# Kernel optimization log

Hardware: AMD Instinct MI355X
Metric: run time of the kernel (lower is better)

The kernel has to match this reference:

```python
import jax, jax.numpy as jnp
import numpy as np

N, E, D = 10000, 160000, 512


def gcn_conv(x, src, dst, W, b):
    # GCNConv (PyG default): linear -> sym-normalized aggregation with self-loops -> +bias
    n = x.shape[0]
    h = x @ W  # [N, D]
    loop = jnp.arange(n)
    s = jnp.concatenate([src, loop])
    d = jnp.concatenate([dst, loop])
    deg = jax.ops.segment_sum(jnp.ones_like(d, dtype=h.dtype), d, num_segments=n)
    dinv = jnp.where(deg > 0, jax.lax.rsqrt(deg), 0.0)
    norm = dinv[s] * dinv[d]  # [E+N]
    msg = h[s] * norm[:, None]  # [E+N, D]
    out = jax.ops.segment_sum(msg, d, num_segments=n)
    return out + b


def gnn_embed(x, edge_index, Ws, bs):
    src, dst = edge_index[0], edge_index[1]
    h = x
    L = len(Ws)
    for i in range(L):
        h = gcn_conv(h, src, dst, Ws[i], bs[i])
        if i < L - 1:
            h = jax.nn.relu(h)
    return jnp.mean(h, axis=0).reshape(1, -1)  # [1, D]


def setup_inputs() -> dict:
    key = jax.random.key(0)
    ks = jax.random.split(key, 16)
    x1 = jax.random.normal(ks[0], (N, D), dtype=jnp.float32)
    x2 = jax.random.normal(ks[1], (N, D), dtype=jnp.float32)
    edge_index1 = jax.random.randint(ks[2], (2, E), 0, N, dtype=jnp.int64)
    edge_index2 = jax.random.randint(ks[3], (2, E), 0, N, dtype=jnp.int64)
    sc = 1.0 / np.sqrt(D)
    W1 = jax.random.normal(ks[4], (D, D), dtype=jnp.float32) * sc
    W2 = jax.random.normal(ks[5], (D, D), dtype=jnp.float32) * sc
    W3 = jax.random.normal(ks[6], (D, D), dtype=jnp.float32) * sc
    b1 = jnp.zeros((D,), jnp.float32)
    b2 = jnp.zeros((D,), jnp.float32)
    b3 = jnp.zeros((D,), jnp.float32)
    # FCL comparison head: concat(u1,u2) [1,2D] -> Linear(2D,D) -> ReLU -> Linear(D,1) -> sigmoid
    Wf1 = jax.random.normal(ks[7], (2 * D, D), dtype=jnp.float32) * (1.0 / np.sqrt(2 * D))
    bf1 = jnp.zeros((D,), jnp.float32)
    Wf2 = jax.random.normal(ks[8], (D, 1), dtype=jnp.float32) * sc
    bf2 = jnp.zeros((1,), jnp.float32)
    return dict(x1=x1, x2=x2, edge_index1=edge_index1, edge_index2=edge_index2,
                W1=W1, W2=W2, W3=W3, b1=b1, b2=b2, b3=b3,
                Wf1=Wf1, bf1=bf1, Wf2=Wf2, bf2=bf2)


def reference(x1, x2, edge_index1, edge_index2, W1, W2, W3, b1, b2, b3, Wf1, bf1, Wf2, bf2):
    Ws, bs = (W1, W2, W3), (b1, b2, b3)
    u1 = gnn_embed(x1, edge_index1, Ws, bs)  # [1, D]
    u2 = gnn_embed(x2, edge_index2, Ws, bs)  # [1, D]
    z = jnp.concatenate([u1, u2], axis=1)  # [1, 2D]
    h = jax.nn.relu(z @ Wf1 + bf1)
    score = jax.nn.sigmoid(h @ Wf2 + bf2)  # [1, 1]
    return score
```

## Files before the change

kernel.cpp:

```cpp
#include <hip/hip_runtime.h>
#include <math.h>

#define NN 10000
#define NE 160000
#define DD 512
#define MPAD 20096

typedef __attribute__((ext_vector_type(8))) short bf16x8;
typedef __attribute__((ext_vector_type(4))) float f32x4;
typedef __attribute__((ext_vector_type(8))) unsigned short u16x8;

__device__ __forceinline__ unsigned short f2bf(float f) {
    unsigned u = __float_as_uint(f);
    u += 0x7FFFu + ((u >> 16) & 1u);
    return (unsigned short)(u >> 16);
}
__device__ __forceinline__ float bf2f(unsigned short h) {
    return __uint_as_float(((unsigned)h) << 16);
}

#define GLOAD16(g, l) __builtin_amdgcn_global_load_lds( \
    (const __attribute__((address_space(1))) void*)(unsigned long long)(const void*)(g), \
    (__attribute__((address_space(3))) void*)(unsigned)(unsigned long long)(void*)(l), \
    16, 0, 0)

__global__ void k_init(int* cnt, int* cursor, float* u, float* hacc) {
    int i = blockIdx.x * blockDim.x + threadIdx.x;
    if (i < 2 * NN) { cnt[i] = 0; cursor[i] = 0; }
    if (i < 2 * DD) u[i] = 0.f;
    if (i < DD) hacc[i] = 0.f;
}

__global__ void k_count(const int* e1, const int* e2, int* cnt) {
    int i = blockIdx.x * blockDim.x + threadIdx.x;
    if (i < NE) {
        atomicAdd(&cnt[e1[NE + i]], 1);
    } else if (i < 2 * NE) {
        int e = i - NE;
        atomicAdd(&cnt[NN + e2[NE + e]], 1);
    }
}

__global__ void k_dinv(const int* cnt, float* dinv) {
    int i = blockIdx.x * blockDim.x + threadIdx.x;
    if (i < 2 * NN) dinv[i] = rsqrtf((float)(cnt[i] + 1));
}

__global__ void k_scan(const int* cnt, int* offs) {
    int g = blockIdx.x;
    const int* c = cnt + g * NN;
    int* o = offs + g * (NN + 1);
    __shared__ int sums[1024];
    int t = threadIdx.x;
    const int PER = 10;
    int base = t * PER;
    int vals[PER];
    int local = 0;
    #pragma unroll
    for (int j = 0; j < PER; ++j) {
        int idx = base + j;
        int v = (idx < NN) ? c[idx] : 0;
        vals[j] = v; local += v;
    }
    sums[t] = local;
    __syncthreads();
    for (int off = 1; off < 1024; off <<= 1) {
        int v = (t >= off) ? sums[t - off] : 0;
        __syncthreads();
        sums[t] += v;
        __syncthreads();
    }
    int prefix = (t > 0) ? sums[t - 1] : 0;
    #pragma unroll
    for (int j = 0; j < PER; ++j) {
        int idx = base + j;
        if (idx < NN) { o[idx] = prefix; prefix += vals[j]; }
    }
    if (t == 1023) o[NN] = sums[1023];
}

__global__ void k_fill(const int* e1, const int* e2, const int* offs,
                       int* cursor, int* adj) {
    int i = blockIdx.x * blockDim.x + threadIdx.x;
    if (i >= 2 * NE) return;
    int g = (i < NE) ? 0 : 1;
    int e = i - g * NE;
    const int* ei = g ? e2 : e1;
    int s = ei[e];
    int d = ei[NE + e];
    int pos = atomicAdd(&cursor[g * NN + d], 1);
    adj[g * NE + offs[g * (NN + 1) + d] + pos] = s;
}

__global__ void k_cvt_x(const float* __restrict__ x1, const float* __restrict__ x2,
                        unsigned short* __restrict__ xb) {
    long long gid = (long long)blockIdx.x * 256 + threadIdx.x;
    long long i8 = gid * 8;
    if (i8 >= (long long)MPAD * DD) return;
    int row = (int)(i8 >> 9);
    int col = (int)(i8 & 511);
    u16x8 ov;
    if (row < 2 * NN) {
        const float* src = (row < NN) ? (x1 + (size_t)row * DD + col)
                                      : (x2 + (size_t)(row - NN) * DD + col);
        float4 f0 = ((const float4*)src)[0];
        float4 f1 = ((const float4*)src)[1];
        ov[0] = f2bf(f0.x); ov[1] = f2bf(f0.y); ov[2] = f2bf(f0.z); ov[3] = f2bf(f0.w);
        ov[4] = f2bf(f1.x); ov[5] = f2bf(f1.y); ov[6] = f2bf(f1.z); ov[7] = f2bf(f1.w);
    } else {
        #pragma unroll
        for (int j = 0; j < 8; ++j) ov[j] = 0;
    }
    *(u16x8*)(xb + i8) = ov;
}

__global__ void k_cvt_w(const float* __restrict__ W1, const float* __restrict__ W2,
                        const float* __restrict__ W3, unsigned short* __restrict__ Wt) {
    __shared__ float t[32][33];
    const float* W = (blockIdx.z == 0) ? W1 : (blockIdx.z == 1) ? W2 : W3;
    unsigned short* o = Wt + (size_t)blockIdx.z * DD * DD;
    int n0 = blockIdx.x * 32, k0 = blockIdx.y * 32;
    int tx = threadIdx.x, ty = threadIdx.y;
    t[ty][tx] = W[(size_t)(k0 + ty) * DD + n0 + tx];
    __syncthreads();
    o[(size_t)(n0 + ty) * DD + k0 + tx] = f2bf(t[tx][ty]);
}

__global__ __launch_bounds__(256) void k_gemm(const unsigned short* __restrict__ A,
                                              const unsigned short* __restrict__ Bt,
                                              unsigned short* __restrict__ C, int M) {
    __shared__ bf16x8 As[512];
    __shared__ bf16x8 Bs[512];
    int tid = threadIdx.x;
    int lane = tid & 63;
    int wid = tid >> 6;
    int wr = wid >> 1, wc = wid & 1;
    int row0 = blockIdx.x * 128;
    int col0 = blockIdx.y * 128;

    int ch0 = wid * 64 + lane;
    int ch1 = 256 + wid * 64 + lane;
    const unsigned short* gA0 = A + (size_t)(row0 + (ch0 & 127)) * DD + (ch0 >> 7) * 8;
    const unsigned short* gA1 = A + (size_t)(row0 + (ch1 & 127)) * DD + (ch1 >> 7) * 8;
    const unsigned short* gB0 = Bt + (size_t)(col0 + (ch0 & 127)) * DD + (ch0 >> 7) * 8;
    const unsigned short* gB1 = Bt + (size_t)(col0 + (ch1 & 127)) * DD + (ch1 >> 7) * 8;

    int iA[4], iB[4];
    #pragma unroll
    for (int m = 0; m < 4; ++m) {
        iA[m] = (lane >> 4) * 128 + wr * 64 + m * 16 + (lane & 15);
        iB[m] = (lane >> 4) * 128 + wc * 64 + m * 16 + (lane & 15);
    }

    f32x4 acc[4][4];
    #pragma unroll
    for (int m = 0; m < 4; ++m)
        #pragma unroll
        for (int n = 0; n < 4; ++n)
            acc[m][n] = (f32x4){0.f, 0.f, 0.f, 0.f};

    for (int k0 = 0; k0 < DD; k0 += 32) {
        GLOAD16(gA0, &As[wid * 64]);
        GLOAD16(gA1, &As[256 + wid * 64]);
        GLOAD16(gB0, &Bs[wid * 64]);
        GLOAD16(gB1, &Bs[256 + wid * 64]);
        gA0 += 32; gA1 += 32; gB0 += 32; gB1 += 32;
        __syncthreads();
        bf16x8 af[4], bfr[4];
        #pragma unroll
        for (int m = 0; m < 4; ++m) { af[m] = As[iA[m]]; bfr[m] = Bs[iB[m]]; }
        #pragma unroll
        for (int m = 0; m < 4; ++m)
            #pragma unroll
            for (int n = 0; n < 4; ++n)
                acc[m][n] = __builtin_amdgcn_mfma_f32_16x16x32_bf16(af[m], bfr[n], acc[m][n], 0, 0, 0);
        __syncthreads();
    }

    #pragma unroll
    for (int m = 0; m < 4; ++m) {
        int rbase = row0 + wr * 64 + m * 16 + (lane >> 4) * 4;
        #pragma unroll
        for (int n = 0; n < 4; ++n) {
            int col = col0 + wc * 64 + n * 16 + (lane & 15);
            f32x4 v = acc[m][n];
            #pragma unroll
            for (int i = 0; i < 4; ++i) {
                int r = rbase + i;
                if (r < M) C[(size_t)r * DD + col] = f2bf(v[i]);
            }
        }
    }
}

template <bool RELU>
__global__ __launch_bounds__(256) void k_aggc(const unsigned short* __restrict__ h,
                                              const int* __restrict__ adj,
                                              const int* __restrict__ offs,
                                              const float* __restrict__ dinv,
                                              const float* __restrict__ bias,
                                              unsigned short* __restrict__ out) {
    int bid = blockIdx.x;
    int combo = bid & 7;
    int nb = bid >> 3;
    int g = combo >> 2;
    int yc = combo & 3;
    int wid = threadIdx.x >> 6;
    int lane = threadIdx.x & 63;
    int sub = lane >> 4;
    int li = lane & 15;
    int v = nb * 16 + wid * 4 + sub;
    int c = yc * 128 + li * 8;
    int gbase = g * NN;
    const int* o = offs + g * (NN + 1);
    int beg = o[v], end = o[v + 1];
    const int* a = adj + g * NE;
    float dv = dinv[gbase + v];
    const unsigned short* hb = h + c;

    u16x8 hv = *(const u16x8*)(hb + (size_t)(gbase + v) * DD);
    float acc[8];
    #pragma unroll
    for (int j = 0; j < 8; ++j) acc[j] = bf2f(hv[j]) * dv;

    int e = beg;
    for (; e + 4 <= end; e += 4) {
        int s0 = a[e] + gbase, s1 = a[e + 1] + gbase;
        int s2 = a[e + 2] + gbase, s3 = a[e + 3] + gbase;
        u16x8 r0 = *(const u16x8*)(hb + (size_t)s0 * DD);
        u16x8 r1 = *(const u16x8*)(hb + (size_t)s1 * DD);
        u16x8 r2 = *(const u16x8*)(hb + (size_t)s2 * DD);
        u16x8 r3 = *(const u16x8*)(hb + (size_t)s3 * DD);
        float d0 = dinv[s0], d1 = dinv[s1], d2 = dinv[s2], d3 = dinv[s3];
        #pragma unroll
        for (int j = 0; j < 8; ++j) {
            acc[j] = fmaf(bf2f(r0[j]), d0, acc[j]);
            acc[j] = fmaf(bf2f(r1[j]), d1, acc[j]);
            acc[j] = fmaf(bf2f(r2[j]), d2, acc[j]);
            acc[j] = fmaf(bf2f(r3[j]), d3, acc[j]);
        }
    }
    for (; e < end; ++e) {
        int s = a[e] + gbase;
        float ds = dinv[s];
        u16x8 hs = *(const u16x8*)(hb + (size_t)s * DD);
        #pragma unroll
        for (int j = 0; j < 8; ++j) acc[j] = fmaf(bf2f(hs[j]), ds, acc[j]);
    }

    float4 b0 = ((const float4*)(bias + c))[0];
    float4 b1 = ((const float4*)(bias + c))[1];
    float bb[8] = {b0.x, b0.y, b0.z, b0.w, b1.x, b1.y, b1.z, b1.w};
    u16x8 ov;
    #pragma unroll
    for (int j = 0; j < 8; ++j) {
        float x = fmaf(acc[j], dv, bb[j]);
        if (RELU) x = fmaxf(x, 0.f);
        ov[j] = f2bf(x);
    }
    *(u16x8*)(out + (size_t)(gbase + v) * DD + c) = ov;
}

__global__ __launch_bounds__(256) void k_meanpart(const unsigned short* __restrict__ h,
                                                  float* __restrict__ u) {
    __shared__ float sm[4][DD];
    int g = blockIdx.y;
    int chunk = blockIdx.x;
    int wid = threadIdx.x >> 6;
    int lane = threadIdx.x & 63;
    int c = lane * 8;
    const int rows_per = (NN + 127) / 128;
    int r0 = chunk * rows_per;
    int r1 = min(r0 + rows_per, NN);
    float acc[8] = {0.f, 0.f, 0.f, 0.f, 0.f, 0.f, 0.f, 0.f};
    for (int r = r0 + wid; r < r1; r += 4) {
        u16x8 hv = *(const u16x8*)(h + (size_t)(g * NN + r) * DD + c);
        #pragma unroll
        for (int j = 0; j < 8; ++j) acc[j] += bf2f(hv[j]);
    }
    #pragma unroll
    for (int j = 0; j < 8; ++j) sm[wid][c + j] = acc[j];
    __syncthreads();
    if (wid == 0) {
        #pragma unroll
        for (int j = 0; j < 8; ++j) {
            float s = sm[0][c + j] + sm[1][c + j] + sm[2][c + j] + sm[3][c + j];
            atomicAdd(&u[g * DD + c + j], s);
        }
    }
}

__global__ void k_head1(const float* __restrict__ u, const float* __restrict__ Wf1,
                        float* __restrict__ hacc) {
    int t = threadIdx.x;
    int kb = blockIdx.x;
    const float inv = 1.0f / (float)NN;
    float acc = 0.f;
    for (int k = kb * 128; k < kb * 128 + 128; ++k) {
        float z = u[k] * inv;
        acc = fmaf(z, Wf1[(size_t)k * DD + t], acc);
    }
    atomicAdd(&hacc[t], acc);
}

__global__ void k_head2(const float* __restrict__ hacc, const float* __restrict__ bf1,
                        const float* __restrict__ Wf2, const float* __restrict__ bf2,
                        float* __restrict__ outp) {
    __shared__ float red[DD];
    int t = threadIdx.x;
    float hv = fmaxf(hacc[t] + bf1[t], 0.f);
    red[t] = hv * Wf2[t];
    __syncthreads();
    for (int s = DD / 2; s > 0; s >>= 1) {
        if (t < s) red[t] += red[t + s];
        __syncthreads();
    }
    if (t == 0) outp[0] = 1.f / (1.f + expf(-(red[0] + bf2[0])));
}

extern "C" void kernel_launch(void* const* d_in, const int* in_sizes, int n_in,
                              void* d_out, int out_size, void* d_ws, size_t ws_size,
                              hipStream_t stream) {
    const float* x1  = (const float*)d_in[0];
    const float* x2  = (const float*)d_in[1];
    const int*   e1  = (const int*)d_in[2];
    const int*   e2  = (const int*)d_in[3];
    const float* W1  = (const float*)d_in[4];
    const float* W2  = (const float*)d_in[5];
    const float* W3  = (const float*)d_in[6];
    const float* b1  = (const float*)d_in[7];
    const float* b2  = (const float*)d_in[8];
    const float* b3  = (const float*)d_in[9];
    const float* Wf1 = (const float*)d_in[10];
    const float* bf1 = (const float*)d_in[11];
    const float* Wf2 = (const float*)d_in[12];
    const float* bf2 = (const float*)d_in[13];
    float* outp = (float*)d_out;

    char* w = (char*)d_ws;
    unsigned short* xb = (unsigned short*)w; w += (size_t)MPAD * DD * 2;
    unsigned short* hG = (unsigned short*)w; w += (size_t)MPAD * DD * 2;
    unsigned short* hA = (unsigned short*)w; w += (size_t)MPAD * DD * 2;
    unsigned short* Wt = (unsigned short*)w; w += (size_t)3 * DD * DD * 2;
    int*   cnt    = (int*)w;   w += 2 * NN * 4;
    int*   cursor = (int*)w;   w += 2 * NN * 4;
    int*   offs   = (int*)w;   w += 2 * (NN + 1) * 4 + 8;
    int*   adj    = (int*)w;   w += 2 * NE * 4;
    float* dinv   = (float*)w; w += 2 * NN * 4;
    float* u      = (float*)w; w += 2 * DD * 4;
    float* hacc   = (float*)w; w += DD * 4;

    const int M = 2 * NN;

    k_init<<<(2 * NN + 255) / 256, 256, 0, stream>>>(cnt, cursor, u, hacc);
    k_count<<<(2 * NE + 255) / 256, 256, 0, stream>>>(e1, e2, cnt);
    k_dinv<<<(2 * NN + 255) / 256, 256, 0, stream>>>(cnt, dinv);
    k_scan<<<2, 1024, 0, stream>>>(cnt, offs);
    k_fill<<<(2 * NE + 255) / 256, 256, 0, stream>>>(e1, e2, offs, cursor, adj);
    k_cvt_x<<<(MPAD * DD / 8 + 255) / 256, 256, 0, stream>>>(x1, x2, xb);
    k_cvt_w<<<dim3(16, 16, 3), dim3(32, 32), 0, stream>>>(W1, W2, W3, Wt);

    dim3 ggrid(MPAD / 128, DD / 128);
    const int aggGrid = (NN / 16) * 8;

    k_gemm<<<ggrid, 256, 0, stream>>>(xb, Wt, hG, M);
    k_aggc<true><<<aggGrid, 256, 0, stream>>>(hG, adj, offs, dinv, b1, hA);
    k_gemm<<<ggrid, 256, 0, stream>>>(hA, Wt + (size_t)DD * DD, hG, M);
    k_aggc<true><<<aggGrid, 256, 0, stream>>>(hG, adj, offs, dinv, b2, hA);
    k_gemm<<<ggrid, 256, 0, stream>>>(hA, Wt + (size_t)2 * DD * DD, hG, M);
    k_aggc<false><<<aggGrid, 256, 0, stream>>>(hG, adj, offs, dinv, b3, hA);

    k_meanpart<<<dim3(128, 2), 256, 0, stream>>>(hA, u);
    k_head1<<<8, DD, 0, stream>>>(u, Wf1, hacc);
    k_head2<<<1, DD, 0, stream>>>(hacc, bf1, Wf2, bf2, outp);
}
```

Measured before the change: 296.7 us.

## Fuse mean into last aggregation, widen GEMM K-tile, remap blocks per XCD

Several changes at once. The init kernel becomes a memset, dinv is computed inside the scan, and the final mean is fused into the last aggregation, so the last layer's output is never written and re-read. The GEMM doubles its K tile to 64 (fewer barriers), drops the row bound check since the buffer is padded, and remaps the 1D grid so neighbouring tiles share an XCD for L2 reuse. The aggregation gather is unrolled to 8 edges for more loads in flight and uses nontemporal stores. The risks are more LDS and register use, and contention on the per-block atomics in the fused mean.

```diff
diff --git a/kernel.cpp b/kernel.cpp
--- a/kernel.cpp
+++ b/kernel.cpp
@@ -23,13 +23,6 @@
     (const __attribute__((address_space(1))) void*)(unsigned long long)(const void*)(g), \
     (__attribute__((address_space(3))) void*)(unsigned)(unsigned long long)(void*)(l), \
     16, 0, 0)
-
-__global__ void k_init(int* cnt, int* cursor, float* u, float* hacc) {
-    int i = blockIdx.x * blockDim.x + threadIdx.x;
-    if (i < 2 * NN) { cnt[i] = 0; cursor[i] = 0; }
-    if (i < 2 * DD) u[i] = 0.f;
-    if (i < DD) hacc[i] = 0.f;
-}
 
 __global__ void k_count(const int* e1, const int* e2, int* cnt) {
     int i = blockIdx.x * blockDim.x + threadIdx.x;
@@ -41,12 +34,7 @@
     }
 }
 
-__global__ void k_dinv(const int* cnt, float* dinv) {
-    int i = blockIdx.x * blockDim.x + threadIdx.x;
-    if (i < 2 * NN) dinv[i] = rsqrtf((float)(cnt[i] + 1));
-}
-
-__global__ void k_scan(const int* cnt, int* offs) {
+__global__ void k_scan(const int* cnt, int* offs, float* dinv) {
     int g = blockIdx.x;
     const int* c = cnt + g * NN;
     int* o = offs + g * (NN + 1);
@@ -61,6 +49,7 @@
         int idx = base + j;
         int v = (idx < NN) ? c[idx] : 0;
         vals[j] = v; local += v;
+        if (idx < NN) dinv[g * NN + idx] = rsqrtf((float)(v + 1));
     }
     sums[t] = local;
     __syncthreads();
@@ -128,28 +117,35 @@
 
 __global__ __launch_bounds__(256) void k_gemm(const unsigned short* __restrict__ A,
                                               const unsigned short* __restrict__ Bt,
-                                              unsigned short* __restrict__ C, int M) {
-    __shared__ bf16x8 As[512];
-    __shared__ bf16x8 Bs[512];
+                                              unsigned short* __restrict__ C) {
+    __shared__ bf16x8 As[1024];
+    __shared__ bf16x8 Bs[1024];
     int tid = threadIdx.x;
     int lane = tid & 63;
     int wid = tid >> 6;
     int wr = wid >> 1, wc = wid & 1;
-    int row0 = blockIdx.x * 128;
-    int col0 = blockIdx.y * 128;
-
-    int ch0 = wid * 64 + lane;
-    int ch1 = 256 + wid * 64 + lane;
-    const unsigned short* gA0 = A + (size_t)(row0 + (ch0 & 127)) * DD + (ch0 >> 7) * 8;
-    const unsigned short* gA1 = A + (size_t)(row0 + (ch1 & 127)) * DD + (ch1 >> 7) * 8;
-    const unsigned short* gB0 = Bt + (size_t)(col0 + (ch0 & 127)) * DD + (ch0 >> 7) * 8;
-    const unsigned short* gB1 = Bt + (size_t)(col0 + (ch1 & 127)) * DD + (ch1 >> 7) * 8;
-
-    int iA[4], iB[4];
-    #pragma unroll
-    for (int m = 0; m < 4; ++m) {
-        iA[m] = (lane >> 4) * 128 + wr * 64 + m * 16 + (lane & 15);
-        iB[m] = (lane >> 4) * 128 + wc * 64 + m * 16 + (lane & 15);
+
+    int b = blockIdx.x;
+    int xcd = b & 7;
+    int idx = b >> 3;
+    int start = (xcd < 4) ? xcd * 79 : 316 + (xcd - 4) * 78;
+    int gi = start + idx;
+    int rp = gi >> 2, cb = gi & 3;
+    int row0 = rp * 128, col0 = cb * 128;
+
+    const unsigned short* gA[4];
+    const unsigned short* gB[4];
+    bf16x8* lA[4];
+    bf16x8* lB[4];
+    #pragma unroll
+    for (int j = 0; j < 4; ++j) {
+        int t = j * 4 + wid;
+        int row = 64 * (t & 1) + lane;
+        int kb = t >> 1;
+        gA[j] = A + (size_t)(row0 + row) * DD + kb * 8;
+        gB[j] = Bt + (size_t)(col0 + row) * DD + kb * 8;
+        lA[j] = &As[t * 64];
+        lB[j] = &Bs[t * 64];
     }
 
     f32x4 acc[4][4];
@@ -159,21 +155,29 @@
         for (int n = 0; n < 4; ++n)
             acc[m][n] = (f32x4){0.f, 0.f, 0.f, 0.f};
 
-    for (int k0 = 0; k0 < DD; k0 += 32) {
-        GLOAD16(gA0, &As[wid * 64]);
-        GLOAD16(gA1, &As[256 + wid * 64]);
-        GLOAD16(gB0, &Bs[wid * 64]);
-        GLOAD16(gB1, &Bs[256 + wid * 64]);
-        gA0 += 32; gA1 += 32; gB0 += 32; gB1 += 32;
-        __syncthreads();
-        bf16x8 af[4], bfr[4];
-        #pragma unroll
-        for (int m = 0; m < 4; ++m) { af[m] = As[iA[m]]; bfr[m] = Bs[iB[m]]; }
-        #pragma unroll
-        for (int m = 0; m < 4; ++m)
-            #pragma unroll
-            for (int n = 0; n < 4; ++n)
-                acc[m][n] = __builtin_amdgcn_mfma_f32_16x16x32_bf16(af[m], bfr[n], acc[m][n], 0, 0, 0);
+    for (int k0 = 0; k0 < DD; k0 += 64) {
+        #pragma unroll
+        for (int j = 0; j < 4; ++j) GLOAD16(gA[j], lA[j]);
+        #pragma unroll
+        for (int j = 0; j < 4; ++j) GLOAD16(gB[j], lB[j]);
+        #pragma unroll
+        for (int j = 0; j < 4; ++j) { gA[j] += 64; gB[j] += 64; }
+        __syncthreads();
+        #pragma unroll
+        for (int kk = 0; kk < 2; ++kk) {
+            bf16x8 af[4], bfr[4];
+            #pragma unroll
+            for (int m = 0; m < 4; ++m) {
+                int kb = kk * 4 + (lane >> 4);
+                af[m]  = As[kb * 128 + wr * 64 + m * 16 + (lane & 15)];
+                bfr[m] = Bs[kb * 128 + wc * 64 + m * 16 + (lane & 15)];
+            }
+            #pragma unroll
+            for (int m = 0; m < 4; ++m)
+                #pragma unroll
+                for (int n = 0; n < 4; ++n)
+                    acc[m][n] = __builtin_amdgcn_mfma_f32_16x16x32_bf16(af[m], bfr[n], acc[m][n], 0, 0, 0);
+        }
         __syncthreads();
     }
 
@@ -185,21 +189,20 @@
             int col = col0 + wc * 64 + n * 16 + (lane & 15);
             f32x4 v = acc[m][n];
             #pragma unroll
-            for (int i = 0; i < 4; ++i) {
-                int r = rbase + i;
-                if (r < M) C[(size_t)r * DD + col] = f2bf(v[i]);
-            }
-        }
-    }
-}
-
-template <bool RELU>
+            for (int i = 0; i < 4; ++i)
+                C[(size_t)(rbase + i) * DD + col] = f2bf(v[i]);
+        }
+    }
+}
+
+template <bool RELU, bool MEAN>
 __global__ __launch_bounds__(256) void k_aggc(const unsigned short* __restrict__ h,
                                               const int* __restrict__ adj,
                                               const int* __restrict__ offs,
                                               const float* __restrict__ dinv,
                                               const float* __restrict__ bias,
-                                              unsigned short* __restrict__ out) {
+                                              unsigned short* __restrict__ out,
+                                              float* __restrict__ u) {
     int bid = blockIdx.x;
     int combo = bid & 7;
     int nb = bid >> 3;
@@ -224,21 +227,21 @@
     for (int j = 0; j < 8; ++j) acc[j] = bf2f(hv[j]) * dv;
 
     int e = beg;
-    for (; e + 4 <= end; e += 4) {
-        int s0 = a[e] + gbase, s1 = a[e + 1] + gbase;
-        int s2 = a[e + 2] + gbase, s3 = a[e + 3] + gbase;
-        u16x8 r0 = *(const u16x8*)(hb + (size_t)s0 * DD);
-        u16x8 r1 = *(const u16x8*)(hb + (size_t)s1 * DD);
-        u16x8 r2 = *(const u16x8*)(hb + (size_t)s2 * DD);
-        u16x8 r3 = *(const u16x8*)(hb + (size_t)s3 * DD);
-        float d0 = dinv[s0], d1 = dinv[s1], d2 = dinv[s2], d3 = dinv[s3];
-        #pragma unroll
-        for (int j = 0; j < 8; ++j) {
-            acc[j] = fmaf(bf2f(r0[j]), d0, acc[j]);
-            acc[j] = fmaf(bf2f(r1[j]), d1, acc[j]);
-            acc[j] = fmaf(bf2f(r2[j]), d2, acc[j]);
-            acc[j] = fmaf(bf2f(r3[j]), d3, acc[j]);
-        }
+    for (; e + 8 <= end; e += 8) {
+        int s[8];
+        u16x8 r[8];
+        float d[8];
+        #pragma unroll
+        for (int q = 0; q < 8; ++q) s[q] = a[e + q] + gbase;
+        #pragma unroll
+        for (int q = 0; q < 8; ++q) r[q] = *(const u16x8*)(hb + (size_t)s[q] * DD);
+        #pragma unroll
+        for (int q = 0; q < 8; ++q) d[q] = dinv[s[q]];
+        #pragma unroll
+        for (int q = 0; q < 8; ++q)
+            #pragma unroll
+            for (int j = 0; j < 8; ++j)
+                acc[j] = fmaf(bf2f(r[q][j]), d[q], acc[j]);
     }
     for (; e < end; ++e) {
         int s = a[e] + gbase;
@@ -251,42 +254,39 @@
     float4 b0 = ((const float4*)(bias + c))[0];
     float4 b1 = ((const float4*)(bias + c))[1];
     float bb[8] = {b0.x, b0.y, b0.z, b0.w, b1.x, b1.y, b1.z, b1.w};
-    u16x8 ov;
-    #pragma unroll
-    for (int j = 0; j < 8; ++j) {
-        float x = fmaf(acc[j], dv, bb[j]);
-        if (RELU) x = fmaxf(x, 0.f);
-        ov[j] = f2bf(x);
-    }
-    *(u16x8*)(out + (size_t)(gbase + v) * DD + c) = ov;
-}
-
-__global__ __launch_bounds__(256) void k_meanpart(const unsigned short* __restrict__ h,
-                                                  float* __restrict__ u) {
-    __shared__ float sm[4][DD];
-    int g = blockIdx.y;
-    int chunk = blockIdx.x;
-    int wid = threadIdx.x >> 6;
-    int lane = threadIdx.x & 63;
-    int c = lane * 8;
-    const int rows_per = (NN + 127) / 128;
-    int r0 = chunk * rows_per;
-    int r1 = min(r0 + rows_per, NN);
-    float acc[8] = {0.f, 0.f, 0.f, 0.f, 0.f, 0.f, 0.f, 0.f};
-    for (int r = r0 + wid; r < r1; r += 4) {
-        u16x8 hv = *(const u16x8*)(h + (size_t)(g * NN + r) * DD + c);
-        #pragma unroll
-        for (int j = 0; j < 8; ++j) acc[j] += bf2f(hv[j]);
-    }
-    #pragma unroll
-    for (int j = 0; j < 8; ++j) sm[wid][c + j] = acc[j];
-    __syncthreads();
-    if (wid == 0) {
+
+    if (MEAN) {
+        __shared__ float sm[4][128];
+        float x[8];
+        #pragma unroll
+        for (int j = 0; j < 8; ++j) x[j] = fmaf(acc[j], dv, bb[j]);
         #pragma unroll
         for (int j = 0; j < 8; ++j) {
-            float s = sm[0][c + j] + sm[1][c + j] + sm[2][c + j] + sm[3][c + j];
-            atomicAdd(&u[g * DD + c + j], s);
-        }
+            x[j] += __shfl_xor(x[j], 16);
+            x[j] += __shfl_xor(x[j], 32);
+        }
+        if (lane < 16) {
+            #pragma unroll
+            for (int j = 0; j < 8; ++j) sm[wid][li * 8 + j] = x[j];
+        }
+        __syncthreads();
+        if (wid == 0 && lane < 16) {
+            #pragma unroll
+            for (int j = 0; j < 8; ++j) {
+                int cc = li * 8 + j;
+                float s4 = sm[0][cc] + sm[1][cc] + sm[2][cc] + sm[3][cc];
+                atomicAdd(&u[g * DD + yc * 128 + cc], s4);
+            }
+        }
+    } else {
+        u16x8 ov;
+        #pragma unroll
+        for (int j = 0; j < 8; ++j) {
+            float x = fmaf(acc[j], dv, bb[j]);
+            if (RELU) x = fmaxf(x, 0.f);
+            ov[j] = f2bf(x);
+        }
+        __builtin_nontemporal_store(ov, (u16x8*)(out + (size_t)(gbase + v) * DD + c));
     }
 }
 
@@ -342,35 +342,33 @@
     unsigned short* hG = (unsigned short*)w; w += (size_t)MPAD * DD * 2;
     unsigned short* hA = (unsigned short*)w; w += (size_t)MPAD * DD * 2;
     unsigned short* Wt = (unsigned short*)w; w += (size_t)3 * DD * DD * 2;
+    int*   adj    = (int*)w;   w += 2 * NE * 4;
+    int*   offs   = (int*)w;   w += 2 * (NN + 1) * 4 + 8;
+    float* dinv   = (float*)w; w += 2 * NN * 4;
+    char*  zbase  = w;
     int*   cnt    = (int*)w;   w += 2 * NN * 4;
     int*   cursor = (int*)w;   w += 2 * NN * 4;
-    int*   offs   = (int*)w;   w += 2 * (NN + 1) * 4 + 8;
-    int*   adj    = (int*)w;   w += 2 * NE * 4;
-    float* dinv   = (float*)w; w += 2 * NN * 4;
     float* u      = (float*)w; w += 2 * DD * 4;
     float* hacc   = (float*)w; w += DD * 4;
-
-    const int M = 2 * NN;
-
-    k_init<<<(2 * NN + 255) / 256, 256, 0, stream>>>(cnt, cursor, u, hacc);
+    size_t zeroBytes = (size_t)(w - zbase);
+
+    hipMemsetAsync(zbase, 0, zeroBytes, stream);
     k_count<<<(2 * NE + 255) / 256, 256, 0, stream>>>(e1, e2, cnt);
-    k_dinv<<<(2 * NN + 255) / 256, 256, 0, stream>>>(cnt, dinv);
-    k_scan<<<2, 1024, 0, stream>>>(cnt, offs);
+    k_scan<<<2, 1024, 0, stream>>>(cnt, offs, dinv);
     k_fill<<<(2 * NE + 255) / 256, 256, 0, stream>>>(e1, e2, offs, cursor, adj);
     k_cvt_x<<<(MPAD * DD / 8 + 255) / 256, 256, 0, stream>>>(x1, x2, xb);
     k_cvt_w<<<dim3(16, 16, 3), dim3(32, 32), 0, stream>>>(W1, W2, W3, Wt);
 
-    dim3 ggrid(MPAD / 128, DD / 128);
+    const int ggrid = (MPAD / 128) * (DD / 128);
     const int aggGrid = (NN / 16) * 8;
 
-    k_gemm<<<ggrid, 256, 0, stream>>>(xb, Wt, hG, M);
-    k_aggc<true><<<aggGrid, 256, 0, stream>>>(hG, adj, offs, dinv, b1, hA);
-    k_gemm<<<ggrid, 256, 0, stream>>>(hA, Wt + (size_t)DD * DD, hG, M);
-    k_aggc<true><<<aggGrid, 256, 0, stream>>>(hG, adj, offs, dinv, b2, hA);
-    k_gemm<<<ggrid, 256, 0, stream>>>(hA, Wt + (size_t)2 * DD * DD, hG, M);
-    k_aggc<false><<<aggGrid, 256, 0, stream>>>(hG, adj, offs, dinv, b3, hA);
-
-    k_meanpart<<<dim3(128, 2), 256, 0, stream>>>(hA, u);
+    k_gemm<<<ggrid, 256, 0, stream>>>(xb, Wt, hG);
+    k_aggc<true, false><<<aggGrid, 256, 0, stream>>>(hG, adj, offs, dinv, b1, hA, u);
+    k_gemm<<<ggrid, 256, 0, stream>>>(hA, Wt + (size_t)DD * DD, hG);
+    k_aggc<true, false><<<aggGrid, 256, 0, stream>>>(hG, adj, offs, dinv, b2, hA, u);
+    k_gemm<<<ggrid, 256, 0, stream>>>(hA, Wt + (size_t)2 * DD * DD, hG);
+    k_aggc<false, true><<<aggGrid, 256, 0, stream>>>(hG, adj, offs, dinv, b3, hA, u);
+
     k_head1<<<8, DD, 0, stream>>>(u, Wf1, hacc);
     k_head2<<<1, DD, 0, stream>>>(hacc, bf1, Wf2, bf2, outp);
 }
```

Result: slower. 397.1 us (+33.8%).
